# Performance work log

Measured on AMD Instinct MI355X. Metric: run time of the kernel, lower is better.

## Reference

```python
import jax, jax.numpy as jnp
import numpy as np
from jax import lax

TEMPERATURE = 34.0
PAD = 1

def setup_inputs() -> dict:
    key = jax.random.key(0)
    ks = jax.random.split(key, 6)
    B, C, H, W = 16, 256, 64, 64
    K, O, kk, hidden = 4, 256, 3, int(256 * 0.25) + 1
    return {
        "x": jax.random.normal(ks[0], (B, C, H, W), jnp.float32),
        "w_fc1": jax.random.normal(ks[1], (hidden, C), jnp.float32) * 0.05,
        "w_fc2": jax.random.normal(ks[2], (K, hidden), jnp.float32) * 0.05,
        "b_fc2": jax.random.normal(ks[3], (K,), jnp.float32) * 0.05,
        "weight": jax.random.normal(ks[4], (K, O, C, kk, kk), jnp.float32) * 0.05,
        "bias": jax.random.normal(ks[5], (K, O), jnp.float32) * 0.05,
    }

def reference(x, w_fc1, w_fc2, b_fc2, weight, bias):
    # attention2d: global avg pool -> 1x1 conv -> relu -> 1x1 conv -> softmax(logits/T)
    pooled = jnp.mean(x, axis=(2, 3))                       # [B, C]
    h = jax.nn.relu(pooled @ w_fc1.T)                       # [B, hidden]
    logits = h @ w_fc2.T + b_fc2                            # [B, K]
    att = jax.nn.softmax(logits / TEMPERATURE, axis=1)      # [B, K]

    K = weight.shape[0]
    # per-sample aggregated kernels/bias
    agg_w = jnp.einsum('bk,koihw->boihw', att, weight)      # [B, O, C, k, k]
    agg_b = att @ bias                                      # [B, O]

    def conv_one(xi, wi):
        # xi: [C, H, W], wi: [O, C, k, k]
        return lax.conv_general_dilated(
            xi[None], wi, window_strides=(1, 1),
            padding=[(PAD, PAD), (PAD, PAD)],
            dimension_numbers=('NCHW', 'OIHW', 'NCHW'))[0]

    out = jax.vmap(conv_one)(x, agg_w)                      # [B, O, H, W]
    return out + agg_b[:, :, None, None]
```

## Files before the change

### kernel.cpp

```cpp
#include <hip/hip_runtime.h>
#include <math.h>

constexpr int B   = 16;
constexpr int C   = 256;
constexpr int H   = 64;
constexpr int W   = 64;
constexpr int K   = 4;
constexpr int O   = 256;
constexpr int HID = 65;
constexpr float TEMP = 34.0f;

typedef __bf16 bf16x8 __attribute__((ext_vector_type(8)));
typedef float  f32x16 __attribute__((ext_vector_type(16)));
typedef unsigned short ushort_t;

__device__ inline ushort_t f2bf(float f) {
    union { float f; unsigned u; } v; v.f = f;
    unsigned u = v.u;
    u += 0x7FFF + ((u >> 16) & 1);
    return (ushort_t)(u >> 16);
}

__device__ inline void gl2lds16(const void* g, void* l) {
    __builtin_amdgcn_global_load_lds(
        (const __attribute__((address_space(1))) unsigned int*)g,
        (__attribute__((address_space(3))) unsigned int*)l, 16, 0, 0);
}

__global__ void tp_kernel(const float* __restrict__ x,
                          ushort_t* __restrict__ xT,
                          float* __restrict__ pooled,
                          float* __restrict__ part,
                          int mode) {
    const int ci = blockIdx.x, yg = blockIdx.y, b = blockIdx.z;
    const int tid = threadIdx.x;
    const int lane = tid & 63;

    __shared__ ushort_t t2[8 * 1154];
    __shared__ float pool_l[16];
    if (tid < 16) pool_l[tid] = 0.f;
    __syncthreads();

    const float* xbase = x + ((size_t)b * C + ci * 16) * (H * W);

    #pragma unroll
    for (int j = 0; j < 8; ++j) {
        const int idx = j * 256 + tid;
        const int xq = idx & 15;
        const int y8 = (idx >> 4) & 7;
        const int c  = idx >> 7;
        float4 v = *(const float4*)(xbase + ((size_t)c * H + (yg * 8 + y8)) * W + xq * 4);
        float s = (v.x + v.y) + (v.z + v.w);
        s += __shfl_xor(s, 1, 64);
        s += __shfl_xor(s, 2, 64);
        s += __shfl_xor(s, 4, 64);
        s += __shfl_xor(s, 8, 64);
        if ((lane & 15) == 0) atomicAdd(&pool_l[c], s);
        ushort_t* d = &t2[y8 * 1154 + (xq * 4) * 18 + c];
        d[0]  = f2bf(v.x);
        d[18] = f2bf(v.y);
        d[36] = f2bf(v.z);
        d[54] = f2bf(v.w);
    }
    __syncthreads();

    #pragma unroll
    for (int q = 0; q < 4; ++q) {
        const int e = q * 256 + tid;
        const int y8 = e >> 7, col = (e >> 1) & 63, half = e & 1;
        const ushort_t* s0 = &t2[y8 * 1154 + col * 18 + half * 8];
        uint4 vv;
        vv.x = *(const unsigned*)(s0 + 0);
        vv.y = *(const unsigned*)(s0 + 2);
        vv.z = *(const unsigned*)(s0 + 4);
        vv.w = *(const unsigned*)(s0 + 6);
        size_t go = (((size_t)(b * 16 + ci) * 64) + (yg * 8 + y8)) * 1024
                  + col * 16 + half * 8;
        *(uint4*)(xT + go) = vv;
    }
    if (mode) {
        if (tid < 16)
            part[(((size_t)(b * 16 + ci)) * 8 + yg) * 16 + tid] = pool_l[tid];
    } else {
        if (tid < 16)
            atomicAdd(&pooled[b * C + ci * 16 + tid], pool_l[tid] * (1.0f / (H * W)));
    }
}

__global__ void attention_kernel(const float* __restrict__ pooled,
                                 const float* __restrict__ part,
                                 const float* __restrict__ w_fc1,
                                 const float* __restrict__ w_fc2,
                                 const float* __restrict__ b_fc2,
                                 float* __restrict__ att,
                                 int mode) {
    const int b = blockIdx.x;
    const int tid = threadIdx.x;
    __shared__ float pool_s[C];
    __shared__ float h_s[HID];
    __shared__ float logit_s[K];

    if (mode) {
        for (int i = tid; i < C; i += blockDim.x) {
            const int ci = i >> 4, cc = i & 15;
            const float* p = part + (((size_t)(b * 16 + ci)) * 8) * 16 + cc;
            float s = 0.f;
            #pragma unroll
            for (int yg = 0; yg < 8; ++yg) s += p[yg * 16];
            pool_s[i] = s * (1.0f / (H * W));
        }
    } else {
        for (int i = tid; i < C; i += blockDim.x) pool_s[i] = pooled[b * C + i];
    }
    __syncthreads();
    for (int j = tid; j < HID; j += blockDim.x) {
        const float* wr = w_fc1 + (size_t)j * C;
        float s = 0.f;
        #pragma unroll 4
        for (int c = 0; c < C; ++c) s += pool_s[c] * wr[c];
        h_s[j] = fmaxf(s, 0.f);
    }
    __syncthreads();
    if (tid < K) {
        const float* wr = w_fc2 + (size_t)tid * HID;
        float s = b_fc2[tid];
        for (int j = 0; j < HID; ++j) s += h_s[j] * wr[j];
        logit_s[tid] = s * (1.0f / TEMP);
    }
    __syncthreads();
    if (tid == 0) {
        float m = fmaxf(fmaxf(logit_s[0], logit_s[1]), fmaxf(logit_s[2], logit_s[3]));
        float e0 = expf(logit_s[0] - m), e1 = expf(logit_s[1] - m);
        float e2 = expf(logit_s[2] - m), e3 = expf(logit_s[3] - m);
        float inv = 1.0f / (e0 + e1 + e2 + e3);
        att[b * K + 0] = e0 * inv; att[b * K + 1] = e1 * inv;
        att[b * K + 2] = e2 * inv; att[b * K + 3] = e3 * inv;
    }
}

__global__ void wagg_kernel(const float* __restrict__ weight,
                            const float* __restrict__ att,
                            ushort_t* __restrict__ wagg_sw) {
    const int ci = blockIdx.x;
    const int mi = blockIdx.y;
    const int tid = threadIdx.x;
    const int lane = tid & 63;
    const int wid  = tid >> 6;

    __shared__ float lds_w[4 * 32 * 145];
    __shared__ float att_s[B * K];

    if (tid < B * K) att_s[tid] = att[tid];

    for (int idx = tid; idx < 128 * 36; idx += 256) {
        const int seg = idx / 36;
        const int off = idx - seg * 36;
        const int k = seg >> 5, o = seg & 31;
        const float4 v = *(const float4*)(weight
            + ((size_t)(k * O + mi * 32 + o) * C + ci * 16) * 9 + off * 4);
        float* d = &lds_w[seg * 145 + off * 4];
        d[0] = v.x; d[1] = v.y; d[2] = v.z; d[3] = v.w;
    }
    __syncthreads();

    const int o_l = lane & 31;
    const int cc0 = (lane >> 5) * 8;
    for (int task = wid; task < B * 9; task += 4) {
        const int b = task / 9, t = task - b * 9;
        const float a0 = att_s[b * K + 0], a1 = att_s[b * K + 1];
        const float a2 = att_s[b * K + 2], a3 = att_s[b * K + 3];
        union { ushort_t u[8]; uint4 v; } pk;
        #pragma unroll
        for (int j = 0; j < 8; ++j) {
            const int m = (cc0 + j) * 9 + t;
            pk.u[j] = f2bf(a0 * lds_w[(0 * 32 + o_l) * 145 + m]
                         + a1 * lds_w[(1 * 32 + o_l) * 145 + m]
                         + a2 * lds_w[(2 * 32 + o_l) * 145 + m]
                         + a3 * lds_w[(3 * 32 + o_l) * 145 + m]);
        }
        size_t idx = ((((size_t)b * 16 + ci) * 9 + t) * 8 + mi) * 512 + lane * 8;
        *(uint4*)&wagg_sw[idx] = pk.v;
    }
}

__global__ __launch_bounds__(256, 2)
void conv_mfma_kernel(const ushort_t* __restrict__ xT,
                      const ushort_t* __restrict__ wagg_sw,
                      const float* __restrict__ bias,
                      const float* __restrict__ att,
                      float* __restrict__ out) {
    const int b  = blockIdx.x;
    const int yt = blockIdx.y;
    const int oz = blockIdx.z;
    const int y0 = yt * 4;

    const int tid  = threadIdx.x;
    const int lane = tid & 63;
    const int wid  = tid >> 6;
    const int n16  = lane & 31;
    const int khalf = lane >> 5;

    __shared__ __align__(16) ushort_t A_lds[9 * 4 * 512];
    __shared__ __align__(16) ushort_t x_lds[6 * 1056];

    for (int i = tid; i < 6 * 1056; i += 256) x_lds[i] = 0;

    f32x16 acc[4][2];
    #pragma unroll
    for (int a = 0; a < 4; ++a)
        #pragma unroll
        for (int ni = 0; ni < 2; ++ni)
            acc[a][ni] = (f32x16)(0.f);

    for (int ci = 0; ci < 16; ++ci) {
        __syncthreads();

        for (int i = wid; i < 36; i += 4) {
            const int t = i >> 2, a = i & 3;
            const ushort_t* g = wagg_sw
                + ((((size_t)b * 16 + ci) * 9 + t) * 8 + (oz * 4 + a)) * 512 + lane * 8;
            gl2lds16(g, &A_lds[(t * 4 + a) * 512]);
        }
        for (int r = wid; r < 6; r += 4) {
            const int y = y0 - 1 + r;
            if ((unsigned)y < (unsigned)H) {
                const ushort_t* gr = xT + (((size_t)(b * 16 + ci) * 64 + y) * 1024);
                #pragma unroll
                for (int h = 0; h < 2; ++h)
                    gl2lds16(gr + lane * 16 + h * 8,
                             &x_lds[r * 1056 + h * 528 + 8]);
            }
        }

        __syncthreads();

        #pragma unroll
        for (int dy = 0; dy < 3; ++dy) {
            const int r = wid + dy;
            #pragma unroll
            for (int dx = 0; dx < 3; ++dx) {
                const int t = dy * 3 + dx;
                bf16x8 bf[2];
                #pragma unroll
                for (int ni = 0; ni < 2; ++ni)
                    bf[ni] = *(const bf16x8*)&x_lds[r * 1056 + khalf * 528
                              + (ni * 32 + n16 + dx) * 8];
                #pragma unroll
                for (int a = 0; a < 4; ++a) {
                    bf16x8 af = *(const bf16x8*)&A_lds[(t * 4 + a) * 512 + lane * 8];
                    acc[a][0] = __builtin_amdgcn_mfma_f32_32x32x16_bf16(af, bf[0], acc[a][0], 0, 0, 0);
                    acc[a][1] = __builtin_amdgcn_mfma_f32_32x32x16_bf16(af, bf[1], acc[a][1], 0, 0, 0);
                }
            }
        }
    }

    __syncthreads();
    float* aggb = (float*)A_lds;
    if (tid < 128) {
        const int o = oz * 128 + tid;
        aggb[tid] = att[b * K + 0] * bias[0 * O + o] + att[b * K + 1] * bias[1 * O + o]
                  + att[b * K + 2] * bias[2 * O + o] + att[b * K + 3] * bias[3 * O + o];
    }
    __syncthreads();

    const int y = y0 + wid;
    #pragma unroll
    for (int a = 0; a < 4; ++a) {
        #pragma unroll
        for (int ni = 0; ni < 2; ++ni) {
            #pragma unroll
            for (int reg = 0; reg < 16; ++reg) {
                const int row = (reg & 3) + 8 * (reg >> 2) + 4 * khalf;
                const int ol  = a * 32 + row;
                out[(((size_t)b * O + oz * 128 + ol) * H + y) * W + ni * 32 + n16]
                    = acc[a][ni][reg] + aggb[ol];
            }
        }
    }
}

__global__ void pool_kernel(const float* __restrict__ x, float* __restrict__ pooled) {
    const int bc = blockIdx.x;
    const float4* p4 = (const float4*)(x + (size_t)bc * (H * W));
    const int tid = threadIdx.x;
    float s = 0.f;
    #pragma unroll
    for (int i = 0; i < (H * W / 4) / 256; ++i) {
        float4 v = p4[tid + i * 256];
        s += (v.x + v.y) + (v.z + v.w);
    }
    #pragma unroll
    for (int off = 32; off > 0; off >>= 1) s += __shfl_down(s, off, 64);
    __shared__ float red[4];
    if ((tid & 63) == 0) red[tid >> 6] = s;
    __syncthreads();
    if (tid == 0) pooled[bc] = ((red[0] + red[1]) + (red[2] + red[3])) * (1.0f / (H * W));
}

constexpr int TILE_H = 32;
constexpr int TILE_W = 64;
constexpr int CCF = 4, OT = 8, PX = 8;
constexpr int XS_STRIDE = TILE_W + 3;

__global__ __launch_bounds__(256, 2)
void conv_kernel(const float* __restrict__ x, const float* __restrict__ weight,
                 const float* __restrict__ bias, const float* __restrict__ att,
                 float* __restrict__ out) {
    const int tile_y = blockIdx.x, o0 = blockIdx.y * OT, b = blockIdx.z;
    const int tid = threadIdx.x, tx = tid & 7, ty = tid >> 3, ty0 = tile_y * TILE_H;
    __shared__ __align__(16) float xs[CCF][TILE_H + 2][XS_STRIDE];
    __shared__ __align__(16) float ws_s[OT][CCF][12];
    const float a0 = att[b * K + 0], a1 = att[b * K + 1];
    const float a2 = att[b * K + 2], a3 = att[b * K + 3];
    float acc[OT][PX];
    #pragma unroll
    for (int o = 0; o < OT; ++o)
        #pragma unroll
        for (int p = 0; p < PX; ++p) acc[o][p] = 0.f;
    const float* xb = x + (size_t)b * C * H * W;
    constexpr int X_ELEMS = CCF * (TILE_H + 2) * (TILE_W + 2);
    constexpr int W_ELEMS = OT * CCF * 9;
    for (int c0 = 0; c0 < C; c0 += CCF) {
        __syncthreads();
        for (int idx = tid; idx < X_ELEMS; idx += 256) {
            int cc = idx / ((TILE_H + 2) * (TILE_W + 2));
            int rem = idx - cc * ((TILE_H + 2) * (TILE_W + 2));
            int r = rem / (TILE_W + 2), col = rem - r * (TILE_W + 2);
            int gy = ty0 - 1 + r, gx = col - 1;
            float v = 0.f;
            if ((unsigned)gy < (unsigned)H && (unsigned)gx < (unsigned)W)
                v = xb[((size_t)(c0 + cc) * H + gy) * W + gx];
            xs[cc][r][col] = v;
        }
        for (int idx = tid; idx < W_ELEMS; idx += 256) {
            int o = idx / (CCF * 9), rem = idx - o * (CCF * 9);
            int cc = rem / 9, tap = rem - cc * 9;
            size_t base = ((size_t)(o0 + o) * C + (c0 + cc)) * 9 + tap;
            ws_s[o][cc][tap] = a0 * weight[base] + a1 * weight[(size_t)1 * O * C * 9 + base]
                             + a2 * weight[(size_t)2 * O * C * 9 + base]
                             + a3 * weight[(size_t)3 * O * C * 9 + base];
        }
        __syncthreads();
        #pragma unroll
        for (int cc = 0; cc < CCF; ++cc) {
            float xv[3][10];
            #pragma unroll
            for (int dy = 0; dy < 3; ++dy)
                #pragma unroll
                for (int j = 0; j < 10; ++j) xv[dy][j] = xs[cc][ty + dy][8 * tx + j];
            #pragma unroll
            for (int o = 0; o < OT; ++o) {
                float4 w0 = *(const float4*)&ws_s[o][cc][0];
                float4 w1 = *(const float4*)&ws_s[o][cc][4];
                float w8 = ws_s[o][cc][8];
                #pragma unroll
                for (int p = 0; p < PX; ++p) {
                    float s = acc[o][p];
                    s = fmaf(xv[0][p + 0], w0.x, s); s = fmaf(xv[0][p + 1], w0.y, s);
                    s = fmaf(xv[0][p + 2], w0.z, s); s = fmaf(xv[1][p + 0], w0.w, s);
                    s = fmaf(xv[1][p + 1], w1.x, s); s = fmaf(xv[1][p + 2], w1.y, s);
                    s = fmaf(xv[2][p + 0], w1.z, s); s = fmaf(xv[2][p + 1], w1.w, s);
                    s = fmaf(xv[2][p + 2], w8, s);
                    acc[o][p] = s;
                }
            }
        }
    }
    const int oy = ty0 + ty, ox = 8 * tx;
    #pragma unroll
    for (int o = 0; o < OT; ++o) {
        float ab = a0 * bias[0 * O + o0 + o] + a1 * bias[1 * O + o0 + o]
                 + a2 * bias[2 * O + o0 + o] + a3 * bias[3 * O + o0 + o];
        float4 v0 = make_float4(acc[o][0] + ab, acc[o][1] + ab, acc[o][2] + ab, acc[o][3] + ab);
        float4 v1 = make_float4(acc[o][4] + ab, acc[o][5] + ab, acc[o][6] + ab, acc[o][7] + ab);
        float* op = out + (((size_t)b * O + (o0 + o)) * H + oy) * W + ox;
        *(float4*)(op) = v0; *(float4*)(op + 4) = v1;
    }
}

extern "C" void kernel_launch(void* const* d_in, const int* in_sizes, int n_in,
                              void* d_out, int out_size, void* d_ws, size_t ws_size,
                              hipStream_t stream) {
    const float* x      = (const float*)d_in[0];
    const float* w_fc1  = (const float*)d_in[1];
    const float* w_fc2  = (const float*)d_in[2];
    const float* b_fc2  = (const float*)d_in[3];
    const float* weight = (const float*)d_in[4];
    const float* bias   = (const float*)d_in[5];
    float* out = (float*)d_out;

    float* pooled = (float*)d_ws;
    float* att    = pooled + B * C;
    ushort_t* wagg_sw = (ushort_t*)((char*)d_ws + 32 * 1024);
    const size_t wagg_bytes = (size_t)B * 16 * 9 * 8 * 512 * 2;
    ushort_t* xT = (ushort_t*)((char*)wagg_sw + wagg_bytes);
    const size_t xT_bytes = (size_t)B * 16 * 64 * 64 * 16 * 2;
    float* part = (float*)((char*)xT + xT_bytes);
    const size_t part_bytes = (size_t)B * 16 * 8 * 16 * sizeof(float);
    const size_t needed  = 32 * 1024 + wagg_bytes + xT_bytes;
    const size_t needed2 = needed + part_bytes;

    if (ws_size >= needed2) {
        tp_kernel<<<dim3(16, 8, 16), dim3(256), 0, stream>>>(x, xT, pooled, part, 1);
        attention_kernel<<<dim3(B), dim3(128), 0, stream>>>(pooled, part, w_fc1, w_fc2, b_fc2, att, 1);
        wagg_kernel<<<dim3(16, 8), dim3(256), 0, stream>>>(weight, att, wagg_sw);
        conv_mfma_kernel<<<dim3(B, 16, 2), dim3(256), 0, stream>>>(xT, wagg_sw, bias, att, out);
    } else if (ws_size >= needed) {
        hipMemsetAsync(pooled, 0, B * C * sizeof(float), stream);
        tp_kernel<<<dim3(16, 8, 16), dim3(256), 0, stream>>>(x, xT, pooled, pooled, 0);
        attention_kernel<<<dim3(B), dim3(128), 0, stream>>>(pooled, pooled, w_fc1, w_fc2, b_fc2, att, 0);
        wagg_kernel<<<dim3(16, 8), dim3(256), 0, stream>>>(weight, att, wagg_sw);
        conv_mfma_kernel<<<dim3(B, 16, 2), dim3(256), 0, stream>>>(xT, wagg_sw, bias, att, out);
    } else {
        pool_kernel<<<dim3(B * C), dim3(256), 0, stream>>>(x, pooled);
        attention_kernel<<<dim3(B), dim3(128), 0, stream>>>(pooled, pooled, w_fc1, w_fc2, b_fc2, att, 0);
        conv_kernel<<<dim3(H / TILE_H, O / OT, B), dim3(256), 0, stream>>>(x, weight, bias, att, out);
    }
}
```

Baseline: 220.2 us.

## Double-buffer conv LDS staging and halve output-channel tile per block

The MFMA conv kernel now double-buffers its LDS tiles for weights and input rows. It prefetches the next channel chunk with async global-to-LDS loads while computing the current one, using a fixed count of loads per wave so a vmcnt wait can be used. Each block now covers 64 output channels instead of 128, doubling the grid along z. This is meant to hide global load latency and improve occupancy and parallelism. The trade-off is that each input tile is reloaded by twice as many blocks, and dummy loads are issued to keep the per-wave load count uniform.

```diff
diff --git a/kernel.cpp b/kernel.cpp
--- a/kernel.cpp
+++ b/kernel.cpp
@@ -200,39 +200,56 @@
     const int n16  = lane & 31;
     const int khalf = lane >> 5;
 
-    __shared__ __align__(16) ushort_t A_lds[9 * 4 * 512];
-    __shared__ __align__(16) ushort_t x_lds[6 * 1056];
-
-    for (int i = tid; i < 6 * 1056; i += 256) x_lds[i] = 0;
-
-    f32x16 acc[4][2];
-    #pragma unroll
-    for (int a = 0; a < 4; ++a)
+    __shared__ __align__(16) ushort_t A_lds[2][18 * 512];
+    __shared__ __align__(16) ushort_t x_lds[2][6 * 1056];
+    __shared__ __align__(16) ushort_t dump_lds[512];
+    __shared__ float aggb[64];
+
+    for (int i = tid; i < 2 * 6 * 1056; i += 256) ((ushort_t*)x_lds)[i] = 0;
+    __syncthreads();
+
+    auto stage = [&](int ci, int buf) {
+        const ushort_t* Ab = wagg_sw
+            + (((size_t)(b * 16 + ci) * 9) * 8 + oz * 2) * 512 + lane * 8;
+        const ushort_t* xb = xT + ((size_t)(b * 16 + ci) * 64) * 1024;
+        #pragma unroll
+        for (int k = 0; k < 8; ++k) {
+            const int s = wid + 4 * k;
+            if (s < 18) {
+                const int t = s >> 1, a = s & 1;
+                gl2lds16(Ab + (size_t)(t * 8 + a) * 512, &A_lds[buf][s * 512]);
+            } else if (s < 30) {
+                const int j = s - 18, r = j >> 1, h = j & 1;
+                const int y = y0 - 1 + r;
+                const bool ok = (unsigned)y < (unsigned)H;
+                gl2lds16(xb + (size_t)(ok ? y : 0) * 1024 + lane * 16 + h * 8,
+                         ok ? (void*)&x_lds[buf][r * 1056 + h * 528 + 8]
+                            : (void*)&dump_lds[0]);
+            } else {
+                gl2lds16(Ab, &dump_lds[0]);
+            }
+        }
+    };
+
+    f32x16 acc[2][2];
+    #pragma unroll
+    for (int a = 0; a < 2; ++a)
         #pragma unroll
         for (int ni = 0; ni < 2; ++ni)
             acc[a][ni] = (f32x16)(0.f);
 
+    stage(0, 0);
+
     for (int ci = 0; ci < 16; ++ci) {
-        __syncthreads();
-
-        for (int i = wid; i < 36; i += 4) {
-            const int t = i >> 2, a = i & 3;
-            const ushort_t* g = wagg_sw
-                + ((((size_t)b * 16 + ci) * 9 + t) * 8 + (oz * 4 + a)) * 512 + lane * 8;
-            gl2lds16(g, &A_lds[(t * 4 + a) * 512]);
-        }
-        for (int r = wid; r < 6; r += 4) {
-            const int y = y0 - 1 + r;
-            if ((unsigned)y < (unsigned)H) {
-                const ushort_t* gr = xT + (((size_t)(b * 16 + ci) * 64 + y) * 1024);
-                #pragma unroll
-                for (int h = 0; h < 2; ++h)
-                    gl2lds16(gr + lane * 16 + h * 8,
-                             &x_lds[r * 1056 + h * 528 + 8]);
-            }
-        }
-
-        __syncthreads();
+        const int cur = ci & 1;
+        if (ci < 15) {
+            stage(ci + 1, cur ^ 1);
+            asm volatile("s_waitcnt vmcnt(8)" ::: "memory");
+        } else {
+            asm volatile("s_waitcnt vmcnt(0)" ::: "memory");
+        }
+        __builtin_amdgcn_s_barrier();
+        asm volatile("" ::: "memory");
 
         #pragma unroll
         for (int dy = 0; dy < 3; ++dy) {
@@ -240,25 +257,24 @@
             #pragma unroll
             for (int dx = 0; dx < 3; ++dx) {
                 const int t = dy * 3 + dx;
-                bf16x8 bf[2];
+                bf16x8 bf0 = *(const bf16x8*)&x_lds[cur][r * 1056 + khalf * 528
+                              + (n16 + dx) * 8];
+                bf16x8 bf1 = *(const bf16x8*)&x_lds[cur][r * 1056 + khalf * 528
+                              + (32 + n16 + dx) * 8];
                 #pragma unroll
-                for (int ni = 0; ni < 2; ++ni)
-                    bf[ni] = *(const bf16x8*)&x_lds[r * 1056 + khalf * 528
-                              + (ni * 32 + n16 + dx) * 8];
-                #pragma unroll
-                for (int a = 0; a < 4; ++a) {
-                    bf16x8 af = *(const bf16x8*)&A_lds[(t * 4 + a) * 512 + lane * 8];
-                    acc[a][0] = __builtin_amdgcn_mfma_f32_32x32x16_bf16(af, bf[0], acc[a][0], 0, 0, 0);
-                    acc[a][1] = __builtin_amdgcn_mfma_f32_32x32x16_bf16(af, bf[1], acc[a][1], 0, 0, 0);
+                for (int a = 0; a < 2; ++a) {
+                    bf16x8 af = *(const bf16x8*)&A_lds[cur][(t * 2 + a) * 512 + lane * 8];
+                    acc[a][0] = __builtin_amdgcn_mfma_f32_32x32x16_bf16(af, bf0, acc[a][0], 0, 0, 0);
+                    acc[a][1] = __builtin_amdgcn_mfma_f32_32x32x16_bf16(af, bf1, acc[a][1], 0, 0, 0);
                 }
             }
         }
-    }
-
-    __syncthreads();
-    float* aggb = (float*)A_lds;
-    if (tid < 128) {
-        const int o = oz * 128 + tid;
+        asm volatile("" ::: "memory");
+        __builtin_amdgcn_s_barrier();
+    }
+
+    if (tid < 64) {
+        const int o = oz * 64 + tid;
         aggb[tid] = att[b * K + 0] * bias[0 * O + o] + att[b * K + 1] * bias[1 * O + o]
                   + att[b * K + 2] * bias[2 * O + o] + att[b * K + 3] * bias[3 * O + o];
     }
@@ -266,14 +282,14 @@
 
     const int y = y0 + wid;
     #pragma unroll
-    for (int a = 0; a < 4; ++a) {
+    for (int a = 0; a < 2; ++a) {
         #pragma unroll
         for (int ni = 0; ni < 2; ++ni) {
             #pragma unroll
             for (int reg = 0; reg < 16; ++reg) {
                 const int row = (reg & 3) + 8 * (reg >> 2) + 4 * khalf;
                 const int ol  = a * 32 + row;
-                out[(((size_t)b * O + oz * 128 + ol) * H + y) * W + ni * 32 + n16]
+                out[(((size_t)b * O + oz * 64 + ol) * H + y) * W + ni * 32 + n16]
                     = acc[a][ni][reg] + aggb[ol];
             }
         }
@@ -405,13 +421,13 @@
         tp_kernel<<<dim3(16, 8, 16), dim3(256), 0, stream>>>(x, xT, pooled, part, 1);
         attention_kernel<<<dim3(B), dim3(128), 0, stream>>>(pooled, part, w_fc1, w_fc2, b_fc2, att, 1);
         wagg_kernel<<<dim3(16, 8), dim3(256), 0, stream>>>(weight, att, wagg_sw);
-        conv_mfma_kernel<<<dim3(B, 16, 2), dim3(256), 0, stream>>>(xT, wagg_sw, bias, att, out);
+        conv_mfma_kernel<<<dim3(B, 16, 4), dim3(256), 0, stream>>>(xT, wagg_sw, bias, att, out);
     } else if (ws_size >= needed) {
         hipMemsetAsync(pooled, 0, B * C * sizeof(float), stream);
         tp_kernel<<<dim3(16, 8, 16), dim3(256), 0, stream>>>(x, xT, pooled, pooled, 0);
         attention_kernel<<<dim3(B), dim3(128), 0, stream>>>(pooled, pooled, w_fc1, w_fc2, b_fc2, att, 0);
         wagg_kernel<<<dim3(16, 8), dim3(256), 0, stream>>>(weight, att, wagg_sw);
-        conv_mfma_kernel<<<dim3(B, 16, 2), dim3(256), 0, stream>>>(xT, wagg_sw, bias, att, out);
+        conv_mfma_kernel<<<dim3(B, 16, 4), dim3(256), 0, stream>>>(xT, wagg_sw, bias, att, out);
     } else {
         pool_kernel<<<dim3(B * C), dim3(256), 0, stream>>>(x, pooled);
         attention_kernel<<<dim3(B), dim3(128), 0, stream>>>(pooled, pooled, w_fc1, w_fc2, b_fc2, att, 0);
```

Result: no change. 224.1 us (+1.8%).
